# Performance work log

Measured on AMD Instinct MI355X. Metric: run time of the kernel, lower is better.

Reference implementation:

```python
import jax, jax.numpy as jnp
import numpy as np

QMAX = 7.0   # int4 symmetric, narrow range [-7, 7] per weight; acts use [-8, 7]
QMIN = -8.0

def _ste_quant(v, scale, qmin, qmax):
    """Symmetric per-tensor fake-quant with straight-through estimator."""
    s = jax.lax.stop_gradient(scale)
    q = jnp.clip(jnp.round(v / s), qmin, qmax) * s
    return v + jax.lax.stop_gradient(q - v)


def setup_inputs() -> dict:
    key = jax.random.key(0)
    k1, k2, k3 = jax.random.split(key, 3)
    d_model, vocab = 1024, 50257
    x = jax.random.normal(k1, (2, 1024, d_model), jnp.float32)
    W = jax.random.normal(k2, (vocab, d_model), jnp.float32) * 0.02
    b = jax.random.normal(k3, (vocab,), jnp.float32) * 0.01
    return {"x": x, "W": W, "b": b}


def reference(x, W, b):
    # Activation quant: 4-bit signed, per-tensor scale from max-abs stats
    sx = jnp.max(jnp.abs(x)) / QMAX
    xq = _ste_quant(x, sx, QMIN, QMAX)
    # Weight quant: 4-bit signed per-tensor
    sw = jnp.max(jnp.abs(W)) / QMAX
    wq = _ste_quant(W, sw, QMIN, QMAX)
    # Int32 bias: quantized at the accumulator scale sx*sw (range huge -> round only)
    sb = jax.lax.stop_gradient(sx * sw)
    bq = b + jax.lax.stop_gradient(jnp.round(b / sb) * sb - b)
    # Quantized GEMM with int32-style accumulation, expressed as dequantized matmul
    logits = jnp.einsum('bsd,vd->bsv', xq, wq) + bq  # [B, S, vocab]
    return jax.nn.log_softmax(logits, axis=-1)
```

## Files before the change

kernel.cpp:

```cpp
#include <hip/hip_runtime.h>
#include <hip/hip_bf16.h>

#define N_VOCAB 50257
#define NBC     786
#define N_PAD   50304
#define D_K     1024
#define M_ROWS  2048
#define MT      32
#define GEMM_BLOCKS (NBC * MT)
#define PER_XCD     (GEMM_BLOCKS/8)

typedef __attribute__((ext_vector_type(4))) int i32x4;

__device__ inline void async_copy16(const void* g, void* l) {
  auto* gp = (const __attribute__((address_space(1))) unsigned int*)g;
  auto* lp = (__attribute__((address_space(3))) unsigned int*)l;
  __builtin_amdgcn_global_load_lds(gp, lp, 16, 0, 0);
}

__device__ inline signed char qint(float v, float s) {
  float q = fminf(fmaxf(rintf(v / s), -8.f), 7.f);
  return (signed char)(int)q;
}

__global__ void absmax2_kernel(const float4* __restrict__ x, int nx4,
                               const float4* __restrict__ Wp, int nw4,
                               unsigned* __restrict__ amax) {
  const bool isx = blockIdx.x < 512;
  const float4* p = isx ? x : Wp;
  const int n4 = isx ? nx4 : nw4;
  const int b0 = isx ? blockIdx.x : blockIdx.x - 512;
  const int nb = isx ? 512 : (gridDim.x - 512);
  float m = 0.f;
  for (int i = b0 * blockDim.x + threadIdx.x; i < n4; i += nb * blockDim.x) {
    float4 v = p[i];
    m = fmaxf(m, fmaxf(fmaxf(fabsf(v.x), fabsf(v.y)),
                       fmaxf(fabsf(v.z), fabsf(v.w))));
  }
#pragma unroll
  for (int off = 32; off; off >>= 1) m = fmaxf(m, __shfl_xor(m, off));
  __shared__ float red[4];
  int tid = threadIdx.x;
  if ((tid & 63) == 0) red[tid >> 6] = m;
  __syncthreads();
  if (tid == 0) {
    m = fmaxf(fmaxf(red[0], red[1]), fmaxf(red[2], red[3]));
    atomicMax(&amax[isx ? 0 : 1], __float_as_uint(m));
  }
}

__global__ void quant_kernel(const float4* __restrict__ x,
                             const float4* __restrict__ Wp,
                             const float* __restrict__ b,
                             char4* __restrict__ qx, char4* __restrict__ qw,
                             float* __restrict__ bq,
                             const unsigned* __restrict__ amax) {
  const int bid = blockIdx.x;
  const int tid = threadIdx.x;
  const int nw4 = (N_VOCAB * D_K) / 4;
  if (bid < 2048) {
    int i = bid * 256 + tid;
    float s = __uint_as_float(amax[0]) * (1.0f / 7.0f);
    float4 v = x[i];
    char4 q;
    q.x = qint(v.x, s); q.y = qint(v.y, s);
    q.z = qint(v.z, s); q.w = qint(v.w, s);
    qx[i] = q;
  } else if (bid < 2048 + 50304) {
    int i = (bid - 2048) * 256 + tid;
    char4 q = {0, 0, 0, 0};
    if (i < nw4) {
      float s = __uint_as_float(amax[1]) * (1.0f / 7.0f);
      float4 v = Wp[i];
      q.x = qint(v.x, s); q.y = qint(v.y, s);
      q.z = qint(v.z, s); q.w = qint(v.w, s);
    }
    qw[i] = q;
  } else {
    int i = (bid - (2048 + 50304)) * 256 + tid;
    if (i < N_PAD) {
      float v = 0.f;
      if (i < N_VOCAB) {
        float sb = (__uint_as_float(amax[0]) * (1.0f / 7.0f)) *
                   (__uint_as_float(amax[1]) * (1.0f / 7.0f));
        v = rintf(b[i] / sb) * sb;
      }
      bq[i] = v;
    }
  }
}

__global__ __launch_bounds__(64, 2) void gemm_kernel(
    const signed char* __restrict__ qx,
    const signed char* __restrict__ qw,
    const float* __restrict__ bq,
    const unsigned* __restrict__ amax,
    float* __restrict__ outp,
    float* __restrict__ pmax,
    float* __restrict__ psum)
{
  constexpr int BK = 64;
  constexpr int NT = D_K / BK;
  __shared__ __align__(16) signed char sA[2][64 * BK];
  __shared__ __align__(16) signed char sB[2][64 * BK];

  const int l = threadIdx.x & 63;

  const int bid = blockIdx.x;
  const int vb = (bid & 7) * PER_XCD + (bid >> 3);
  const int nb = vb >> 5;
  const int m0 = (vb & 31) * 64;
  const int n0 = nb * 64;

  const float sx = __uint_as_float(amax[0]) * (1.0f / 7.0f);
  const float sw = __uint_as_float(amax[1]) * (1.0f / 7.0f);
  const float scale = sx * sw;

  i32x4 acc[4][4] = {};

  const int srow = l >> 2;
  const int scol = ((l & 3) ^ ((l >> 3) & 3)) * 16;

  auto stage = [&](int buf, int kt) {
    int k0 = kt * BK;
#pragma unroll
    for (int c = 0; c < 4; ++c) {
      int row = c * 16 + srow;
      async_copy16(qx + (size_t)(m0 + row) * D_K + k0 + scol,
                   &sA[buf][c * 1024]);
    }
#pragma unroll
    for (int c = 0; c < 4; ++c) {
      int row = c * 16 + srow;
      async_copy16(qw + (size_t)(n0 + row) * D_K + k0 + scol,
                   &sB[buf][c * 1024]);
    }
  };

  stage(0, 0);
  stage(1, 1);

#pragma unroll
  for (int kt = 0; kt < NT; ++kt) {
    const int cur = kt & 1;

    if (kt + 1 < NT)
      asm volatile("s_waitcnt vmcnt(8)" ::: "memory");
    else
      asm volatile("s_waitcnt vmcnt(0)" ::: "memory");
    __builtin_amdgcn_sched_barrier(0);

    i32x4 af[4], bfr[4];
#pragma unroll
    for (int mi = 0; mi < 4; ++mi) {
      int row = mi * 16 + (l & 15);
      int kb = ((l >> 4) ^ ((row >> 1) & 3)) * 16;
      af[mi] = *(const i32x4*)&sA[cur][row * BK + kb];
    }
#pragma unroll
    for (int ni = 0; ni < 4; ++ni) {
      int row = ni * 16 + (l & 15);
      int kb = ((l >> 4) ^ ((row >> 1) & 3)) * 16;
      bfr[ni] = *(const i32x4*)&sB[cur][row * BK + kb];
    }
    asm volatile("s_waitcnt lgkmcnt(0)" ::: "memory");
    __builtin_amdgcn_sched_barrier(0);

    if (kt + 2 < NT) stage(cur, kt + 2);
    __builtin_amdgcn_sched_barrier(0);

#pragma unroll
    for (int mi = 0; mi < 4; ++mi)
#pragma unroll
      for (int ni = 0; ni < 4; ++ni)
        acc[mi][ni] = __builtin_amdgcn_mfma_i32_16x16x64_i8(
            af[mi], bfr[ni], acc[mi][ni], 0, 0, 0);
  }

  bool valid[4];
  float bb[4];
#pragma unroll
  for (int ni = 0; ni < 4; ++ni) {
    int col = n0 + ni * 16 + (l & 15);
    valid[ni] = (col < N_VOCAB);
    bb[ni] = valid[ni] ? bq[col] : 0.f;
  }
  float lg[4][4][4];
#pragma unroll
  for (int mi = 0; mi < 4; ++mi)
#pragma unroll
    for (int ni = 0; ni < 4; ++ni)
#pragma unroll
      for (int r = 0; r < 4; ++r)
        lg[mi][ni][r] = (float)acc[mi][ni][r] * scale + bb[ni];

#pragma unroll
  for (int mi = 0; mi < 4; ++mi)
#pragma unroll
    for (int r = 0; r < 4; ++r) {
      float mval = -3.4e38f;
#pragma unroll
      for (int ni = 0; ni < 4; ++ni)
        if (valid[ni]) mval = fmaxf(mval, lg[mi][ni][r]);
#pragma unroll
      for (int off = 1; off < 16; off <<= 1)
        mval = fmaxf(mval, __shfl_xor(mval, off));
      float s = 0.f;
#pragma unroll
      for (int ni = 0; ni < 4; ++ni)
        if (valid[ni]) s += __expf(lg[mi][ni][r] - mval);
#pragma unroll
      for (int off = 1; off < 16; off <<= 1)
        s += __shfl_xor(s, off);
      if ((l & 15) == 0) {
        int rowg = m0 + mi * 16 + (l >> 4) * 4 + r;
        pmax[(size_t)rowg * NBC + nb] = mval;
        psum[(size_t)rowg * NBC + nb] = s;
      }
    }

#pragma unroll
  for (int mi = 0; mi < 4; ++mi)
#pragma unroll
    for (int r = 0; r < 4; ++r) {
      int rowg = m0 + mi * 16 + (l >> 4) * 4 + r;
      size_t rb = (size_t)rowg * N_VOCAB;
#pragma unroll
      for (int ni = 0; ni < 4; ++ni) {
        if (valid[ni]) {
          int col = n0 + ni * 16 + (l & 15);
          outp[rb + col] = lg[mi][ni][r];
        }
      }
    }
}

__global__ __launch_bounds__(256) void logz_sub_kernel(
    const float* __restrict__ pmax, const float* __restrict__ psum,
    float* __restrict__ out) {
  const int row = blockIdx.x >> 1;
  const int half = blockIdx.x & 1;
  const float* pm = pmax + (size_t)row * NBC;
  const float* ps = psum + (size_t)row * NBC;
  const int tid = threadIdx.x;
  __shared__ float red[9];

  float m = -3.4e38f;
  for (int i = tid; i < NBC; i += 256) m = fmaxf(m, pm[i]);
#pragma unroll
  for (int off = 32; off; off >>= 1) m = fmaxf(m, __shfl_xor(m, off));
  if ((tid & 63) == 0) red[tid >> 6] = m;
  __syncthreads();
  m = fmaxf(fmaxf(red[0], red[1]), fmaxf(red[2], red[3]));

  float s = 0.f;
  for (int i = tid; i < NBC; i += 256) s += ps[i] * __expf(pm[i] - m);
#pragma unroll
  for (int off = 32; off; off >>= 1) s += __shfl_xor(s, off);
  if ((tid & 63) == 0) red[4 + (tid >> 6)] = s;
  __syncthreads();
  if (tid == 0) {
    s = red[4] + red[5] + red[6] + red[7];
    red[8] = m + __logf(s);
  }
  __syncthreads();
  const float lz = red[8];

  const size_t base = (size_t)row * N_VOCAB;
  const int a = (4 - (row & 3)) & 3;
  const int n4 = (N_VOCAB - a) >> 2;
  const int h4 = (n4 + 1) >> 1;
  const int i0 = half * h4;
  const int i1 = min(n4, i0 + h4);
  float4* p = (float4*)(out + base + a);
  for (int i = i0 + tid; i < i1; i += 256) {
    float4 v = p[i];
    v.x -= lz; v.y -= lz; v.z -= lz; v.w -= lz;
    p[i] = v;
  }
  if (half == 0) {
    if (tid < a) out[base + tid] -= lz;
  } else {
    const int done = a + n4 * 4;
    if (tid < N_VOCAB - done) out[base + done + tid] -= lz;
  }
}

extern "C" void kernel_launch(void* const* d_in, const int* in_sizes, int n_in,
                              void* d_out, int out_size, void* d_ws,
                              size_t ws_size, hipStream_t stream) {
  const float* x = (const float*)d_in[0];
  const float* W = (const float*)d_in[1];
  const float* b = (const float*)d_in[2];
  float* out = (float*)d_out;

  char* ws = (char*)d_ws;
  unsigned* amax = (unsigned*)ws;
  float* bq = (float*)(ws + 4096);
  float* pmax = (float*)(ws + (1ull << 20));
  float* psum = (float*)(ws + (8ull << 20));
  signed char* qx = (signed char*)(ws + (15ull << 20));
  signed char* qw = (signed char*)(ws + (17ull << 20));

  hipMemsetAsync(amax, 0, 8, stream);

  const int nx4 = (M_ROWS * D_K) / 4;
  const int nw4 = (N_VOCAB * D_K) / 4;

  absmax2_kernel<<<2560, 256, 0, stream>>>((const float4*)x, nx4,
                                           (const float4*)W, nw4, amax);

  quant_kernel<<<2048 + 50304 + 197, 256, 0, stream>>>(
      (const float4*)x, (const float4*)W, b, (char4*)qx, (char4*)qw, bq, amax);

  gemm_kernel<<<GEMM_BLOCKS, 64, 0, stream>>>(qx, qw, bq, amax, out, pmax,
                                              psum);

  logz_sub_kernel<<<M_ROWS * 2, 256, 0, stream>>>(pmax, psum, out);
}
```

Measured before the change: 631.9 us.

## Load GEMM fragments directly from global into registers, dropping LDS staging

The int8 MFMA GEMM no longer stages A/B tiles through LDS with async global-to-LDS copies. Each lane now loads its 16-byte MFMA fragments straight from global memory into a double-buffered register set, prefetching two K-steps ahead, and raises the MFMA wave priority with s_setprio. Occupancy hint goes from 2 to 3 blocks per CU. This removes LDS round trips and waitcnt barriers, but the global loads are strided (16 rows of 1024-byte stride per fragment), so coalescing and cache reuse now depend on L1/L2 and register pressure rises.

```diff
diff --git a/kernel.cpp b/kernel.cpp
--- a/kernel.cpp
+++ b/kernel.cpp
@@ -11,12 +11,6 @@
 #define PER_XCD     (GEMM_BLOCKS/8)
 
 typedef __attribute__((ext_vector_type(4))) int i32x4;
-
-__device__ inline void async_copy16(const void* g, void* l) {
-  auto* gp = (const __attribute__((address_space(1))) unsigned int*)g;
-  auto* lp = (__attribute__((address_space(3))) unsigned int*)l;
-  __builtin_amdgcn_global_load_lds(gp, lp, 16, 0, 0);
-}
 
 __device__ inline signed char qint(float v, float s) {
   float q = fminf(fmaxf(rintf(v / s), -8.f), 7.f);
@@ -90,7 +84,7 @@
   }
 }
 
-__global__ __launch_bounds__(64, 2) void gemm_kernel(
+__global__ __launch_bounds__(64, 3) void gemm_kernel(
     const signed char* __restrict__ qx,
     const signed char* __restrict__ qw,
     const float* __restrict__ bq,
@@ -101,9 +95,6 @@
 {
   constexpr int BK = 64;
   constexpr int NT = D_K / BK;
-  __shared__ __align__(16) signed char sA[2][64 * BK];
-  __shared__ __align__(16) signed char sB[2][64 * BK];
-
   const int l = threadIdx.x & 63;
 
   const int bid = blockIdx.x;
@@ -112,70 +103,48 @@
   const int m0 = (vb & 31) * 64;
   const int n0 = nb * 64;
 
+  const signed char* pa = qx + (size_t)(m0 + (l & 15)) * D_K + (l >> 4) * 16;
+  const signed char* pb = qw + (size_t)(n0 + (l & 15)) * D_K + (l >> 4) * 16;
+
+  i32x4 acc[4][4] = {};
+  i32x4 fa[2][4], fb[2][4];
+
+#pragma unroll
+  for (int i = 0; i < 4; ++i) {
+    fa[0][i] = *(const i32x4*)(pa + i * (16 * D_K));
+    fb[0][i] = *(const i32x4*)(pb + i * (16 * D_K));
+  }
+#pragma unroll
+  for (int i = 0; i < 4; ++i) {
+    fa[1][i] = *(const i32x4*)(pa + i * (16 * D_K) + BK);
+    fb[1][i] = *(const i32x4*)(pb + i * (16 * D_K) + BK);
+  }
+
+#pragma unroll
+  for (int kt = 0; kt < NT; ++kt) {
+    const int s = kt & 1;
+
+    __builtin_amdgcn_s_setprio(1);
+#pragma unroll
+    for (int mi = 0; mi < 4; ++mi)
+#pragma unroll
+      for (int ni = 0; ni < 4; ++ni)
+        acc[mi][ni] = __builtin_amdgcn_mfma_i32_16x16x64_i8(
+            fa[s][mi], fb[s][ni], acc[mi][ni], 0, 0, 0);
+    __builtin_amdgcn_s_setprio(0);
+
+    if (kt + 2 < NT) {
+#pragma unroll
+      for (int i = 0; i < 4; ++i) {
+        fa[s][i] = *(const i32x4*)(pa + i * (16 * D_K) + (kt + 2) * BK);
+        fb[s][i] = *(const i32x4*)(pb + i * (16 * D_K) + (kt + 2) * BK);
+      }
+    }
+  }
+
   const float sx = __uint_as_float(amax[0]) * (1.0f / 7.0f);
   const float sw = __uint_as_float(amax[1]) * (1.0f / 7.0f);
   const float scale = sx * sw;
-
-  i32x4 acc[4][4] = {};
-
-  const int srow = l >> 2;
-  const int scol = ((l & 3) ^ ((l >> 3) & 3)) * 16;
-
-  auto stage = [&](int buf, int kt) {
-    int k0 = kt * BK;
-#pragma unroll
-    for (int c = 0; c < 4; ++c) {
-      int row = c * 16 + srow;
-      async_copy16(qx + (size_t)(m0 + row) * D_K + k0 + scol,
-                   &sA[buf][c * 1024]);
-    }
-#pragma unroll
-    for (int c = 0; c < 4; ++c) {
-      int row = c * 16 + srow;
-      async_copy16(qw + (size_t)(n0 + row) * D_K + k0 + scol,
-                   &sB[buf][c * 1024]);
-    }
-  };
-
-  stage(0, 0);
-  stage(1, 1);
-
-#pragma unroll
-  for (int kt = 0; kt < NT; ++kt) {
-    const int cur = kt & 1;
-
-    if (kt + 1 < NT)
-      asm volatile("s_waitcnt vmcnt(8)" ::: "memory");
-    else
-      asm volatile("s_waitcnt vmcnt(0)" ::: "memory");
-    __builtin_amdgcn_sched_barrier(0);
-
-    i32x4 af[4], bfr[4];
-#pragma unroll
-    for (int mi = 0; mi < 4; ++mi) {
-      int row = mi * 16 + (l & 15);
-      int kb = ((l >> 4) ^ ((row >> 1) & 3)) * 16;
-      af[mi] = *(const i32x4*)&sA[cur][row * BK + kb];
-    }
-#pragma unroll
-    for (int ni = 0; ni < 4; ++ni) {
-      int row = ni * 16 + (l & 15);
-      int kb = ((l >> 4) ^ ((row >> 1) & 3)) * 16;
-      bfr[ni] = *(const i32x4*)&sB[cur][row * BK + kb];
-    }
-    asm volatile("s_waitcnt lgkmcnt(0)" ::: "memory");
-    __builtin_amdgcn_sched_barrier(0);
-
-    if (kt + 2 < NT) stage(cur, kt + 2);
-    __builtin_amdgcn_sched_barrier(0);
-
-#pragma unroll
-    for (int mi = 0; mi < 4; ++mi)
-#pragma unroll
-      for (int ni = 0; ni < 4; ++ni)
-        acc[mi][ni] = __builtin_amdgcn_mfma_i32_16x16x64_i8(
-            af[mi], bfr[ni], acc[mi][ni], 0, 0, 0);
-  }
 
   bool valid[4];
   float bb[4];
```

Measured after the change: 706.3 us. +11.8%, slower.
